# Kernel tuning notes

Measured on AMD Instinct MI355X. Metric: run time of the kernel, lower is better.

Reference implementation:

```python
import jax, jax.numpy as jnp
import numpy as np

B, S, D, H = 4, 2048, 1024, 16
HD = D // H
SCALE = HD ** -0.5


def setup_inputs() -> dict:
    key = jax.random.key(0)
    ks = jax.random.split(key, 5)
    std = D ** -0.5
    return {
        "x": jax.random.normal(ks[0], (B, S, D), jnp.float32),
        "wq": jax.random.normal(ks[1], (D, D), jnp.float32) * std,
        "bq": jnp.zeros((D,), jnp.float32),
        "wk": jax.random.normal(ks[2], (D, D), jnp.float32) * std,
        "bk": jnp.zeros((D,), jnp.float32),
        "wv": jax.random.normal(ks[3], (D, D), jnp.float32) * std,
        "bv": jnp.zeros((D,), jnp.float32),
        "wo": jax.random.normal(ks[4], (D, D), jnp.float32) * std,
        "bo": jnp.zeros((D,), jnp.float32),
    }


def reference(x, wq, bq, wk, bk, wv, bv, wo, bo):
    # projections; weights stored as [in, out] so y = x @ w + b
    q = (x @ wq + bq).reshape(B, S, H, HD).transpose(0, 2, 1, 3)  # [B,H,S,HD]
    k = (x @ wk + bk).reshape(B, S, H, HD).transpose(0, 2, 1, 3)
    v = (x @ wv + bv).reshape(B, S, H, HD).transpose(0, 2, 1, 3)
    attn = jnp.einsum("bhqd,bhkd->bhqk", q, k) * SCALE  # [B,H,S,S]
    attn = jax.nn.softmax(attn, axis=-1)
    out = jnp.einsum("bhqk,bhkd->bhqd", attn, v)  # [B,H,S,HD]
    out = out.transpose(0, 2, 1, 3).reshape(B, S, D)
    return out @ wo + bo
```

## Files before the change

kernel.cpp:

```cpp
#include <hip/hip_runtime.h>
#include <stdint.h>


typedef __attribute__((ext_vector_type(8))) short bf16x8;
typedef __attribute__((ext_vector_type(4))) short bf16x4;
typedef __attribute__((ext_vector_type(4))) float f32x4;
typedef unsigned short u16;
typedef unsigned int u32;

#define AS1 __attribute__((address_space(1)))
#define AS3 __attribute__((address_space(3)))

#define SCALE_L2E 0.18033688011112042f

__device__ __forceinline__ void gld_lds16(const void* g, void* l) {
  __builtin_amdgcn_global_load_lds((const AS1 void*)g, (AS3 void*)l, 16, 0, 0);
}

__device__ __forceinline__ u16 f2bf(float f) {
  u32 x = __builtin_bit_cast(u32, f);
  x += 0x7fff + ((x >> 16) & 1);
  return (u16)(x >> 16);
}

__device__ __forceinline__ u16 f2bf_fast(float a) {
#if __has_builtin(__builtin_amdgcn_cvt_pk_bf16_f32)
  auto v = __builtin_amdgcn_cvt_pk_bf16_f32(a, a);
  return (u16)(__builtin_bit_cast(u32, v) & 0xffffu);
#else
  return f2bf(a);
#endif
}

__device__ __forceinline__ bf16x4 pack_bf16x4(float a, float b, float c, float d) {
#if __has_builtin(__builtin_amdgcn_cvt_pk_bf16_f32)
  u32 lo = __builtin_bit_cast(u32, __builtin_amdgcn_cvt_pk_bf16_f32(a, b));
  u32 hi = __builtin_bit_cast(u32, __builtin_amdgcn_cvt_pk_bf16_f32(c, d));
#else
  u32 lo = (u32)f2bf(a) | ((u32)f2bf(b) << 16);
  u32 hi = (u32)f2bf(c) | ((u32)f2bf(d) << 16);
#endif
  union { u32 w[2]; bf16x4 v; } u;
  u.w[0] = lo; u.w[1] = hi;
  return u.v;
}

__device__ __forceinline__ f32x4 mfma16(bf16x4 a, bf16x4 b, f32x4 c) {
#if __has_builtin(__builtin_amdgcn_mfma_f32_16x16x16_bf16)
  return __builtin_amdgcn_mfma_f32_16x16x16_bf16(a, b, c, 0, 0, 0);
#else
  return __builtin_amdgcn_mfma_f32_16x16x16bf16_1k(a, b, c, 0, 0, 0);
#endif
}

__device__ __forceinline__ float exp2_fast(float x) {
#if __has_builtin(__builtin_amdgcn_exp2f)
  return __builtin_amdgcn_exp2f(x);
#else
  return exp2f(x);
#endif
}

__global__ __launch_bounds__(256) void convert_x(const float* __restrict__ x,
                                                 u16* __restrict__ xb) {
  int i = (blockIdx.x * 256 + threadIdx.x) * 4;
  float4 v = *(const float4*)(x + i);
  ushort4 o;
  o.x = f2bf(v.x); o.y = f2bf(v.y); o.z = f2bf(v.z); o.w = f2bf(v.w);
  *(ushort4*)(xb + i) = o;
}

__global__ __launch_bounds__(256) void pack_weights(
    const float* __restrict__ wq, const float* __restrict__ wk,
    const float* __restrict__ wv, const float* __restrict__ wo,
    u16* __restrict__ wt_qkv, u16* __restrict__ wt_o) {
  __shared__ float tile[64][65];
  int mat = blockIdx.z;
  const float* src = (mat == 0) ? wq : (mat == 1) ? wk : (mat == 2) ? wv : wo;
  int k0 = blockIdx.y * 64, j0 = blockIdx.x * 64;
  int t = threadIdx.x;
  int lr = t >> 6;
  int lc = t & 63;
#pragma unroll
  for (int it = 0; it < 16; ++it) {
    int r = it * 4 + lr;
    tile[r][lc] = src[(size_t)(k0 + r) * 1024 + j0 + lc];
  }
  __syncthreads();
  u16* dst = (mat == 3) ? wt_o : (wt_qkv + (size_t)mat * 1024 * 1024);
#pragma unroll
  for (int it = 0; it < 16; ++it) {
    int nl = it * 4 + lr;
    float v = tile[lc][nl];
    if (mat == 0) v *= SCALE_L2E;
    dst[(size_t)(j0 + nl) * 1024 + k0 + lc] = f2bf(v);
  }
}

template <int MODE>
__global__ __launch_bounds__(256, 2) void gemm_bt(
    const u16* __restrict__ A, const u16* __restrict__ Bt,
    const float* __restrict__ bias0, const float* __restrict__ bias1,
    const float* __restrict__ bias2,
    void* __restrict__ out0v, void* __restrict__ out1v, void* __restrict__ out2v) {
  __shared__ u16 lA[128 * 32];
  __shared__ u16 lB[128 * 32];
  const int K = 1024;
  int tid = threadIdx.x;
  int wave = tid >> 6, lane = tid & 63;

  int bid = blockIdx.x;
  int m0, n0;
  if constexpr (MODE == 0) {
    int xcd = bid & 7, j = bid >> 3;
    n0 = (xcd * 3 + j % 3) * 128;
    m0 = (j / 3) * 128;
  } else {
    n0 = (bid & 7) * 128;
    m0 = (bid >> 3) * 128;
  }
  int wm = (wave & 1) * 64, wn = (wave >> 1) * 64;

  f32x4 acc[4][4];
#pragma unroll
  for (int i = 0; i < 4; ++i)
#pragma unroll
    for (int j = 0; j < 4; ++j) acc[i][j] = f32x4{0.f, 0.f, 0.f, 0.f};

  int srow = lane >> 2;
  int scol = (lane & 3) * 8;

  for (int k0 = 0; k0 < K; k0 += 32) {
#pragma unroll
    for (int c = 0; c < 2; ++c) {
      int rbase = wave * 32 + c * 16;
      gld_lds16(A + (size_t)(m0 + rbase + srow) * K + k0 + scol, lA + rbase * 32);
      gld_lds16(Bt + (size_t)(n0 + rbase + srow) * K + k0 + scol, lB + rbase * 32);
    }
    __syncthreads();
    bf16x8 af[4], bfr[4];
#pragma unroll
    for (int mt = 0; mt < 4; ++mt)
      af[mt] = *(const bf16x8*)(lA + (wm + mt * 16 + (lane & 15)) * 32 + (lane >> 4) * 8);
#pragma unroll
    for (int nt = 0; nt < 4; ++nt)
      bfr[nt] = *(const bf16x8*)(lB + (wn + nt * 16 + (lane & 15)) * 32 + (lane >> 4) * 8);
#pragma unroll
    for (int mt = 0; mt < 4; ++mt)
#pragma unroll
      for (int nt = 0; nt < 4; ++nt)
        acc[mt][nt] = __builtin_amdgcn_mfma_f32_16x16x32_bf16(af[mt], bfr[nt], acc[mt][nt], 0, 0, 0);
    __syncthreads();
  }

  int rbase0 = m0 + wm + (lane >> 4) * 4;
  int cbase = n0 + wn + (lane & 15);
#pragma unroll
  for (int nt = 0; nt < 4; ++nt) {
    int col = cbase + nt * 16;
    if constexpr (MODE == 0) {
      int mat = col >> 10, j = col & 1023;
      const float* bp = (mat == 0) ? bias0 : (mat == 1) ? bias1 : bias2;
      float bv = bp[j];
      if (mat == 0) bv *= SCALE_L2E;
      if (mat == 2) {
        int h = j >> 6, hd = j & 63;
        u16* base = (u16*)out2v;
#pragma unroll
        for (int mt = 0; mt < 4; ++mt) {
          int row0 = rbase0 + mt * 16;
          int b = row0 >> 11, s = row0 & 2047;
          int ci = s >> 6, sg = (s >> 2) & 15;
          int slot = (hd + 4 * sg) & 63;
          size_t off = (size_t)(b * 16 + h) * 131072 + ci * 4096 + sg * 256 + slot * 4;
          ushort4 pk;
          pk.x = f2bf_fast(acc[mt][nt][0] + bv);
          pk.y = f2bf_fast(acc[mt][nt][1] + bv);
          pk.z = f2bf_fast(acc[mt][nt][2] + bv);
          pk.w = f2bf_fast(acc[mt][nt][3] + bv);
          *(ushort4*)(base + off) = pk;
        }
      } else {
        u16* base = (mat == 0) ? (u16*)out0v : (u16*)out1v;
#pragma unroll
        for (int mt = 0; mt < 4; ++mt)
#pragma unroll
          for (int r = 0; r < 4; ++r) {
            int row = rbase0 + mt * 16 + r;
            base[(size_t)row * 1024 + j] = f2bf_fast(acc[mt][nt][r] + bv);
          }
      }
    } else {
      float bv = bias0[col];
      float* o = (float*)out0v;
#pragma unroll
      for (int mt = 0; mt < 4; ++mt)
#pragma unroll
        for (int r = 0; r < 4; ++r) {
          int row = rbase0 + mt * 16 + r;
          o[(size_t)row * 1024 + col] = acc[mt][nt][r] + bv;
        }
    }
  }
}

__global__ __launch_bounds__(512, 4) void flash_attn(
    const u16* __restrict__ Q, const u16* __restrict__ Kb,
    const u16* __restrict__ Vg, u16* __restrict__ ctx) {
  __shared__ u16 lK[2][64 * 32];
  __shared__ u16 lV[4096];
  int tid = threadIdx.x, wave = tid >> 6, lane = tid & 63;

  int F = blockIdx.x;
  int xcd = F & 7, idx = F >> 3;
  int bh = xcd * 8 + (idx >> 3);
  int q0 = (idx & 7) * 256;
  int b = bh >> 4, h = bh & 15;
  const u16* Qp = Q + (size_t)b * 2048 * 1024 + h * 64;
  const u16* Kp = Kb + (size_t)b * 2048 * 1024 + h * 64;
  const u16* Vp = Vg + (size_t)bh * 131072;

  int c = lane & 15, g = lane >> 4;

  bf16x8 qf[2][2];
#pragma unroll
  for (int t = 0; t < 2; ++t) {
    const u16* qrow = Qp + (size_t)(q0 + wave * 32 + t * 16 + c) * 1024 + g * 8;
    qf[t][0] = *(const bf16x8*)qrow;
    qf[t][1] = *(const bf16x8*)(qrow + 32);
  }

  float lsum[2] = {0.f, 0.f};
  f32x4 o[2][4];
#pragma unroll
  for (int t = 0; t < 2; ++t)
#pragma unroll
    for (int dt = 0; dt < 4; ++dt) o[t][dt] = f32x4{0.f, 0.f, 0.f, 0.f};

  int srow = lane >> 2;
  int schunk = (((lane & 3) ^ ((lane >> 3) & 3)) * 8);
  int rsw = (c >> 1) & 3;
  int kk_w = wave & 1;
  int rb = wave >> 1;
  int stg_row = rb * 16 + srow;
  int vrot = c + 4 * g;

  for (int s0 = 0; s0 < 2048; s0 += 64) {
    gld_lds16(Kp + (size_t)(s0 + stg_row) * 1024 + kk_w * 32 + schunk,
              lK[kk_w] + rb * 512);
    gld_lds16(Vp + (size_t)s0 * 64 + wave * 512 + lane * 8, lV + wave * 512);
    __syncthreads();

#pragma unroll
    for (int st = 0; st < 4; ++st) {
      bf16x8 kf0 = *(const bf16x8*)(lK[0] + (st * 16 + c) * 32 + (g ^ rsw) * 8);
      bf16x8 kf1 = *(const bf16x8*)(lK[1] + (st * 16 + c) * 32 + (g ^ rsw) * 8);

      bf16x4 pf[2];
#pragma unroll
      for (int t = 0; t < 2; ++t) {
        f32x4 sa = __builtin_amdgcn_mfma_f32_16x16x32_bf16(kf0, qf[t][0],
                       f32x4{0.f, 0.f, 0.f, 0.f}, 0, 0, 0);
        sa = __builtin_amdgcn_mfma_f32_16x16x32_bf16(kf1, qf[t][1], sa, 0, 0, 0);
        float p0 = exp2_fast(sa[0]), p1 = exp2_fast(sa[1]);
        float p2 = exp2_fast(sa[2]), p3 = exp2_fast(sa[3]);
        lsum[t] += (p0 + p1) + (p2 + p3);
        pf[t] = pack_bf16x4(p0, p1, p2, p3);
      }

      int sg = st * 4 + g;
      int rotb = (vrot + 16 * st) & 63;
#pragma unroll
      for (int dt = 0; dt < 4; ++dt) {
        bf16x4 vf = *(const bf16x4*)(lV + sg * 256 + (((rotb + dt * 16) & 63) << 2));
#pragma unroll
        for (int t = 0; t < 2; ++t)
          o[t][dt] = mfma16(vf, pf[t], o[t][dt]);
      }
    }
    __syncthreads();
  }

#pragma unroll
  for (int t = 0; t < 2; ++t) {
    float rs = lsum[t];
    rs += __shfl_xor(rs, 16);
    rs += __shfl_xor(rs, 32);
    float inv = 1.0f / fmaxf(rs, 1e-30f);
    int q = q0 + wave * 32 + t * 16 + c;
    size_t rowbase = ((size_t)(b * 2048 + q) * 16 + h) * 64;
#pragma unroll
    for (int dt = 0; dt < 4; ++dt) {
      ushort4 pk;
      pk.x = f2bf_fast(o[t][dt][0] * inv);
      pk.y = f2bf_fast(o[t][dt][1] * inv);
      pk.z = f2bf_fast(o[t][dt][2] * inv);
      pk.w = f2bf_fast(o[t][dt][3] * inv);
      *(ushort4*)(ctx + rowbase + dt * 16 + g * 4) = pk;
    }
  }
}

extern "C" void kernel_launch(void* const* d_in, const int* in_sizes, int n_in,
                              void* d_out, int out_size, void* d_ws, size_t ws_size,
                              hipStream_t stream) {
  const float* x  = (const float*)d_in[0];
  const float* wq = (const float*)d_in[1];
  const float* bq = (const float*)d_in[2];
  const float* wk = (const float*)d_in[3];
  const float* bk = (const float*)d_in[4];
  const float* wv = (const float*)d_in[5];
  const float* bv = (const float*)d_in[6];
  const float* wo = (const float*)d_in[7];
  const float* bo = (const float*)d_in[8];

  u16* ws = (u16*)d_ws;
  u16* xb     = ws;
  u16* wt_qkv = xb + (size_t)8192 * 1024;
  u16* wt_o   = wt_qkv + (size_t)3072 * 1024;
  u16* Qb     = wt_o + (size_t)1024 * 1024;
  u16* Kbuf   = Qb + (size_t)8192 * 1024;
  u16* Vgb    = Kbuf + (size_t)8192 * 1024;
  u16* ctx    = Vgb + (size_t)8192 * 1024;

  convert_x<<<8192, 256, 0, stream>>>(x, xb);
  pack_weights<<<dim3(16, 16, 4), 256, 0, stream>>>(wq, wk, wv, wo, wt_qkv, wt_o);
  gemm_bt<0><<<1536, 256, 0, stream>>>(xb, wt_qkv, bq, bk, bv, Qb, Kbuf, Vgb);
  flash_attn<<<512, 512, 0, stream>>>(Qb, Kbuf, Vgb, ctx);
  gemm_bt<1><<<512, 256, 0, stream>>>(ctx, wt_o, bo, nullptr, nullptr,
                                      d_out, nullptr, nullptr);
}
```

Before: 292.4 us.

## Switch flash attention inner loop to 32x32x16 bf16 MFMA tiles

Restructures the attention inner loop so each wave computes a 32x32 score tile with 32x32x16 MFMAs and accumulates P·V with 32x32x16 MFMAs, replacing the 16x16x32 and 16x16x16 instructions. Q fragments, K/V LDS reads and the output write-back are remapped to the new lane layout. The aim is fewer MFMA issues and less LDS fragment traffic per flop through larger tiles with more operand reuse. The trade-off is higher register pressure from 16-wide accumulators and a more complex V gather from the rotated LDS layout.

After: 293.1 us. Within noise of the previous version (+0.2%).

```diff
diff --git a/kernel.cpp b/kernel.cpp
--- a/kernel.cpp
+++ b/kernel.cpp
@@ -5,6 +5,7 @@
 typedef __attribute__((ext_vector_type(8))) short bf16x8;
 typedef __attribute__((ext_vector_type(4))) short bf16x4;
 typedef __attribute__((ext_vector_type(4))) float f32x4;
+typedef __attribute__((ext_vector_type(16))) float f32x16;
 typedef unsigned short u16;
 typedef unsigned int u32;
 
@@ -32,24 +33,11 @@
 #endif
 }
 
-__device__ __forceinline__ bf16x4 pack_bf16x4(float a, float b, float c, float d) {
+__device__ __forceinline__ u32 pk2(float a, float b) {
 #if __has_builtin(__builtin_amdgcn_cvt_pk_bf16_f32)
-  u32 lo = __builtin_bit_cast(u32, __builtin_amdgcn_cvt_pk_bf16_f32(a, b));
-  u32 hi = __builtin_bit_cast(u32, __builtin_amdgcn_cvt_pk_bf16_f32(c, d));
+  return __builtin_bit_cast(u32, __builtin_amdgcn_cvt_pk_bf16_f32(a, b));
 #else
-  u32 lo = (u32)f2bf(a) | ((u32)f2bf(b) << 16);
-  u32 hi = (u32)f2bf(c) | ((u32)f2bf(d) << 16);
-#endif
-  union { u32 w[2]; bf16x4 v; } u;
-  u.w[0] = lo; u.w[1] = hi;
-  return u.v;
-}
-
-__device__ __forceinline__ f32x4 mfma16(bf16x4 a, bf16x4 b, f32x4 c) {
-#if __has_builtin(__builtin_amdgcn_mfma_f32_16x16x16_bf16)
-  return __builtin_amdgcn_mfma_f32_16x16x16_bf16(a, b, c, 0, 0, 0);
-#else
-  return __builtin_amdgcn_mfma_f32_16x16x16bf16_1k(a, b, c, 0, 0, 0);
+  return (u32)f2bf(a) | ((u32)f2bf(b) << 16);
 #endif
 }
 
@@ -59,6 +47,13 @@
 #else
   return exp2f(x);
 #endif
+}
+
+__device__ __forceinline__ f32x16 zero16() {
+  f32x16 z;
+#pragma unroll
+  for (int i = 0; i < 16; ++i) z[i] = 0.f;
+  return z;
 }
 
 __global__ __launch_bounds__(256) void convert_x(const float* __restrict__ x,
@@ -220,30 +215,28 @@
   const u16* Kp = Kb + (size_t)b * 2048 * 1024 + h * 64;
   const u16* Vp = Vg + (size_t)bh * 131072;
 
-  int c = lane & 15, g = lane >> 4;
-
-  bf16x8 qf[2][2];
-#pragma unroll
-  for (int t = 0; t < 2; ++t) {
-    const u16* qrow = Qp + (size_t)(q0 + wave * 32 + t * 16 + c) * 1024 + g * 8;
-    qf[t][0] = *(const bf16x8*)qrow;
-    qf[t][1] = *(const bf16x8*)(qrow + 32);
-  }
-
-  float lsum[2] = {0.f, 0.f};
-  f32x4 o[2][4];
-#pragma unroll
-  for (int t = 0; t < 2; ++t)
-#pragma unroll
-    for (int dt = 0; dt < 4; ++dt) o[t][dt] = f32x4{0.f, 0.f, 0.f, 0.f};
+  int ql = lane & 31;
+  int hi = lane >> 5;
+
+  bf16x8 qf[4];
+  {
+    const u16* qrow = Qp + (size_t)(q0 + wave * 32 + ql) * 1024;
+#pragma unroll
+    for (int kk = 0; kk < 4; ++kk)
+      qf[kk] = *(const bf16x8*)(qrow + kk * 16 + hi * 8);
+  }
+
+  float lsum = 0.f;
+  f32x16 o[2];
+  o[0] = zero16();
+  o[1] = zero16();
 
   int srow = lane >> 2;
   int schunk = (((lane & 3) ^ ((lane >> 3) & 3)) * 8);
-  int rsw = (c >> 1) & 3;
   int kk_w = wave & 1;
   int rb = wave >> 1;
   int stg_row = rb * 16 + srow;
-  int vrot = c + 4 * g;
+  int rkey = ((lane & 15) >> 1) & 3;
 
   for (int s0 = 0; s0 < 2048; s0 += 64) {
     gld_lds16(Kp + (size_t)(s0 + stg_row) * 1024 + kk_w * 32 + schunk,
@@ -252,53 +245,66 @@
     __syncthreads();
 
 #pragma unroll
-    for (int st = 0; st < 4; ++st) {
-      bf16x8 kf0 = *(const bf16x8*)(lK[0] + (st * 16 + c) * 32 + (g ^ rsw) * 8);
-      bf16x8 kf1 = *(const bf16x8*)(lK[1] + (st * 16 + c) * 32 + (g ^ rsw) * 8);
-
-      bf16x4 pf[2];
-#pragma unroll
-      for (int t = 0; t < 2; ++t) {
-        f32x4 sa = __builtin_amdgcn_mfma_f32_16x16x32_bf16(kf0, qf[t][0],
-                       f32x4{0.f, 0.f, 0.f, 0.f}, 0, 0, 0);
-        sa = __builtin_amdgcn_mfma_f32_16x16x32_bf16(kf1, qf[t][1], sa, 0, 0, 0);
-        float p0 = exp2_fast(sa[0]), p1 = exp2_fast(sa[1]);
-        float p2 = exp2_fast(sa[2]), p3 = exp2_fast(sa[3]);
-        lsum[t] += (p0 + p1) + (p2 + p3);
-        pf[t] = pack_bf16x4(p0, p1, p2, p3);
+    for (int sb = 0; sb < 2; ++sb) {
+      bf16x8 kf[4];
+      int krb = (sb * 32 + ql) * 32;
+#pragma unroll
+      for (int kk = 0; kk < 4; ++kk)
+        kf[kk] = *(const bf16x8*)(lK[kk >> 1] + krb + ((((kk & 1) << 1) | hi) ^ rkey) * 8);
+
+      f32x16 sa = zero16();
+#pragma unroll
+      for (int kk = 0; kk < 4; ++kk)
+        sa = __builtin_amdgcn_mfma_f32_32x32x16_bf16(kf[kk], qf[kk], sa, 0, 0, 0);
+
+      float p[16];
+#pragma unroll
+      for (int r = 0; r < 16; ++r) p[r] = exp2_fast(sa[r]);
+      {
+        float a0 = (p[0] + p[1]) + (p[2] + p[3]);
+        float a1 = (p[4] + p[5]) + (p[6] + p[7]);
+        float a2 = (p[8] + p[9]) + (p[10] + p[11]);
+        float a3 = (p[12] + p[13]) + (p[14] + p[15]);
+        lsum += (a0 + a1) + (a2 + a3);
       }
 
-      int sg = st * 4 + g;
-      int rotb = (vrot + 16 * st) & 63;
-#pragma unroll
-      for (int dt = 0; dt < 4; ++dt) {
-        bf16x4 vf = *(const bf16x4*)(lV + sg * 256 + (((rotb + dt * 16) & 63) << 2));
-#pragma unroll
-        for (int t = 0; t < 2; ++t)
-          o[t][dt] = mfma16(vf, pf[t], o[t][dt]);
+#pragma unroll
+      for (int ss = 0; ss < 2; ++ss) {
+        union { u32 w[4]; bf16x8 v; } pu;
+        pu.w[0] = pk2(p[8 * ss + 0], p[8 * ss + 1]);
+        pu.w[1] = pk2(p[8 * ss + 2], p[8 * ss + 3]);
+        pu.w[2] = pk2(p[8 * ss + 4], p[8 * ss + 5]);
+        pu.w[3] = pk2(p[8 * ss + 6], p[8 * ss + 7]);
+        int sgA = sb * 8 + ss * 4 + hi;
+        int sgB = sgA + 2;
+#pragma unroll
+        for (int dh = 0; dh < 2; ++dh) {
+          int d = dh * 32 + ql;
+          union { bf16x4 half_[2]; bf16x8 v; } vu;
+          vu.half_[0] = *(const bf16x4*)(lV + sgA * 256 + (((d + 4 * sgA) & 63) << 2));
+          vu.half_[1] = *(const bf16x4*)(lV + sgB * 256 + (((d + 4 * sgB) & 63) << 2));
+          o[dh] = __builtin_amdgcn_mfma_f32_32x32x16_bf16(vu.v, pu.v, o[dh], 0, 0, 0);
+        }
       }
     }
     __syncthreads();
   }
 
-#pragma unroll
-  for (int t = 0; t < 2; ++t) {
-    float rs = lsum[t];
-    rs += __shfl_xor(rs, 16);
-    rs += __shfl_xor(rs, 32);
-    float inv = 1.0f / fmaxf(rs, 1e-30f);
-    int q = q0 + wave * 32 + t * 16 + c;
-    size_t rowbase = ((size_t)(b * 2048 + q) * 16 + h) * 64;
-#pragma unroll
-    for (int dt = 0; dt < 4; ++dt) {
+  float rs = lsum + __shfl_xor(lsum, 32);
+  float inv = 1.0f / fmaxf(rs, 1e-30f);
+  int q = q0 + wave * 32 + ql;
+  size_t rowbase = ((size_t)(b * 2048 + q) * 16 + h) * 64;
+#pragma unroll
+  for (int dh = 0; dh < 2; ++dh)
+#pragma unroll
+    for (int rr = 0; rr < 4; ++rr) {
       ushort4 pk;
-      pk.x = f2bf_fast(o[t][dt][0] * inv);
-      pk.y = f2bf_fast(o[t][dt][1] * inv);
-      pk.z = f2bf_fast(o[t][dt][2] * inv);
-      pk.w = f2bf_fast(o[t][dt][3] * inv);
-      *(ushort4*)(ctx + rowbase + dt * 16 + g * 4) = pk;
+      pk.x = f2bf_fast(o[dh][4 * rr + 0] * inv);
+      pk.y = f2bf_fast(o[dh][4 * rr + 1] * inv);
+      pk.z = f2bf_fast(o[dh][4 * rr + 2] * inv);
+      pk.w = f2bf_fast(o[dh][4 * rr + 3] * inv);
+      *(ushort4*)(ctx + rowbase + dh * 32 + rr * 8 + hi * 4) = pk;
     }
-  }
 }
 
 extern "C" void kernel_launch(void* const* d_in, const int* in_sizes, int n_in,
```
